# Kernel tuning notes

Hardware: AMD Instinct MI355X
Metric: run time of the kernel (lower is better)

## Reference

```python
import jax, jax.numpy as jnp
import numpy as np

EMBED_DIM = 256
N_HEADS = 1
NORM_FACTOR = float(np.sqrt(EMBED_DIM / N_HEADS))


def setup_inputs() -> dict:
    key = jax.random.key(0)
    ks = jax.random.split(key, 7)
    B, S, E = 4, 4096, EMBED_DIM
    scale = 1.0 / np.sqrt(E)
    x = jax.random.normal(ks[0], (B, S, E), dtype=jnp.float32)
    Wq = jax.random.normal(ks[1], (E, E), dtype=jnp.float32) * scale
    bq = jax.random.normal(ks[2], (E,), dtype=jnp.float32) * 0.01
    Wk = jax.random.normal(ks[3], (E, E), dtype=jnp.float32) * scale
    bk = jax.random.normal(ks[4], (E,), dtype=jnp.float32) * 0.01
    Wv = jax.random.normal(ks[5], (E, E), dtype=jnp.float32) * scale
    bv = jax.random.normal(ks[6], (E,), dtype=jnp.float32) * 0.01
    return {"x": x, "Wq": Wq, "bq": bq, "Wk": Wk, "bk": bk, "Wv": Wv, "bv": bv}


def reference(x, Wq, bq, Wk, bk, Wv, bv):
    # Linear projections (torch Linear: x @ W.T + b; W here stored as [in, out]-equivalent square)
    q = x @ Wq + bq  # [B, S, E]
    k = x @ Wk + bk  # [B, S, E]
    v = x @ Wv + bv  # [B, S, E]
    # Full attention scores [B, S, S], scaled by sqrt(embed_dim / n_heads)
    attn_scores = jnp.einsum('bse,bte->bst', q, k) / NORM_FACTOR
    attn_dist = jax.nn.softmax(attn_scores, axis=-1)
    pooled = jnp.einsum('bst,bte->bse', attn_dist, v)  # [B, S, E]
    return pooled.mean(axis=1, keepdims=True)  # [B, 1, E]
```

## Files before the change

kernel.cpp:

```cpp
#include <hip/hip_runtime.h>
#include <hip/hip_fp8.h>
#include <stdint.h>

#define SS 4096
#define EE 256
#define C2 0.0901684400555602f
#define SCALE1 0x7F7F7F7F
#define ZMAX 8.5f

typedef __bf16 bf16x8 __attribute__((ext_vector_type(8)));
typedef float  f32x4  __attribute__((ext_vector_type(4)));
typedef float  f32x2  __attribute__((ext_vector_type(2)));
typedef int    i32x8  __attribute__((ext_vector_type(8)));

#if __has_builtin(__builtin_amdgcn_exp2f)
#define EXP2(x) __builtin_amdgcn_exp2f(x)
#else
#define EXP2(x) exp2f(x)
#endif
#if __has_builtin(__builtin_amdgcn_rcpf)
#define RCP(x) __builtin_amdgcn_rcpf(x)
#else
#define RCP(x) (1.0f / (x))
#endif

__device__ __forceinline__ uint16_t bf16_rn(float f) {
  uint32_t u = __float_as_uint(f);
  uint32_t r = (u + 0x7fffu + ((u >> 16) & 1u)) >> 16;
  return (uint16_t)r;
}
__device__ __forceinline__ float bf2f(uint16_t h) {
  return __uint_as_float(((uint32_t)h) << 16);
}
__device__ __forceinline__ bf16x8 pack_bf8(float4 a, float4 b) {
  union { bf16x8 v; uint16_t u[8]; } r;
  r.u[0] = bf16_rn(a.x); r.u[1] = bf16_rn(a.y);
  r.u[2] = bf16_rn(a.z); r.u[3] = bf16_rn(a.w);
  r.u[4] = bf16_rn(b.x); r.u[5] = bf16_rn(b.y);
  r.u[6] = bf16_rn(b.z); r.u[7] = bf16_rn(b.w);
  return r.v;
}
__device__ __forceinline__ uint8_t f32_to_e4m3(float x) {
#if __has_builtin(__builtin_amdgcn_cvt_pk_fp8_f32)
  return (uint8_t)(__builtin_amdgcn_cvt_pk_fp8_f32(x, 0.f, 0, false) & 0xff);
#else
  __hip_fp8_e4m3 h(x);
  return (uint8_t)h.__x;
#endif
}
__device__ __forceinline__ uint32_t pack4_e4m3(float a, float b, float c, float d) {
#if __has_builtin(__builtin_amdgcn_cvt_pk_fp8_f32)
  int v = __builtin_amdgcn_cvt_pk_fp8_f32(a, b, 0, false);
  v = __builtin_amdgcn_cvt_pk_fp8_f32(c, d, v, true);
  return (uint32_t)v;
#else
  return (uint32_t)f32_to_e4m3(a) | ((uint32_t)f32_to_e4m3(b) << 8) |
         ((uint32_t)f32_to_e4m3(c) << 16) | ((uint32_t)f32_to_e4m3(d) << 24);
#endif
}
__device__ __forceinline__ float e4m3_f32(uint32_t u) {
  uint32_t bits = ((u & 0x80u) << 24) | ((u & 0x7fu) << 20);
  return __uint_as_float(bits) * 0x1p+120f;
}
__device__ __forceinline__ void decode_fma4(uint32_t w, float rv, float* acc) {
#if __has_builtin(__builtin_amdgcn_cvt_pk_f32_fp8)
  f32x2 lo = __builtin_amdgcn_cvt_pk_f32_fp8((int)w, false);
  f32x2 hi = __builtin_amdgcn_cvt_pk_f32_fp8((int)w, true);
  acc[0] += rv * lo[0]; acc[1] += rv * lo[1];
  acc[2] += rv * hi[0]; acc[3] += rv * hi[1];
#else
  acc[0] += rv * e4m3_f32(w & 0xffu);
  acc[1] += rv * e4m3_f32((w >> 8) & 0xffu);
  acc[2] += rv * e4m3_f32((w >> 16) & 0xffu);
  acc[3] += rv * e4m3_f32(w >> 24);
#endif
}

__device__ __forceinline__ f32x4 mfma16(bf16x8 a, bf16x8 b, f32x4 c) {
  return __builtin_amdgcn_mfma_f32_16x16x32_bf16(a, b, c, 0, 0, 0);
}
__device__ __forceinline__ f32x4 mfma128(i32x8 a, i32x8 b, f32x4 c) {
  return __builtin_amdgcn_mfma_scale_f32_16x16x128_f8f6f4(
      a, b, c, 0 , 0 , 0, SCALE1, 0, SCALE1);
}
__device__ __forceinline__ void pin8(i32x8& v) {
  asm volatile("" : "+v"(v));
}

template<int R>
__device__ __forceinline__ void stage_tile(const uint16_t* gsrc, char* lds, int tid) {
  constexpr int NPER = (R * 32) / 256;
  const int wave = tid >> 6;
  #pragma unroll
  for (int c = 0; c < NPER; ++c) {
    int chunk = c * 256 + tid;
    int r = chunk >> 5;
    int ccl = (chunk & 31) ^ (r & 31);
    const char* gp = (const char*)gsrc + (r * 32 + ccl) * 16;
    char* lp = lds + (c * 256 + wave * 64) * 16;
    __builtin_amdgcn_global_load_lds(
        (const __attribute__((address_space(1))) uint32_t*)(uintptr_t)gp,
        (__attribute__((address_space(3))) uint32_t*)(uintptr_t)lp,
        16, 0, 0);
  }
}
__device__ __forceinline__ bf16x8 read_frag(const char* lds, int row, int cc) {
  int ccp = cc ^ (row & 31);
  return *(const bf16x8*)(lds + (row * 32 + ccp) * 16);
}

__global__ void prep_kernel(const float* __restrict__ Wq, const float* __restrict__ Wk,
                            const float* __restrict__ Wv, uint16_t* __restrict__ wt,
                            float* __restrict__ zbase, float* __restrict__ out) {
  __shared__ float t[64][65];
  const int bid = blockIdx.x, tid = threadIdx.x;
  if (bid >= 48) {
    int idx = (bid - 48) * 256 + tid;
    float4 z = {0.f, 0.f, 0.f, 0.f};
    if (idx < 8192) ((float4*)zbase)[idx] = z;
    else ((float4*)out)[idx - 8192] = z;
    return;
  }
  const int mat = bid >> 4, tt = bid & 15;
  const int ib = (tt >> 2) * 64, ob = (tt & 3) * 64;
  const float* W = (mat == 0) ? Wq : (mat == 1) ? Wk : Wv;
  #pragma unroll
  for (int p = 0; p < 4; ++p) {
    int idx = p * 256 + tid;
    int r = idx >> 4, c4 = idx & 15;
    float4 f = *(const float4*)&W[(size_t)(ib + r) * 256 + ob + c4 * 4];
    t[r][c4 * 4 + 0] = f.x; t[r][c4 * 4 + 1] = f.y;
    t[r][c4 * 4 + 2] = f.z; t[r][c4 * 4 + 3] = f.w;
  }
  __syncthreads();
  #pragma unroll
  for (int p = 0; p < 4; ++p) {
    int idx = p * 256 + tid;
    int o = idx >> 4, i4 = idx & 15;
    ushort4 u;
    u.x = bf16_rn(t[i4 * 4 + 0][o]);
    u.y = bf16_rn(t[i4 * 4 + 1][o]);
    u.z = bf16_rn(t[i4 * 4 + 2][o]);
    u.w = bf16_rn(t[i4 * 4 + 3][o]);
    *(ushort4*)&wt[((size_t)mat * 256 + ob + o) * 256 + ib + i4 * 4] = u;
  }
}

__global__ __launch_bounds__(256, 2) void qkv_kernel(
    const float* __restrict__ x, const uint16_t* __restrict__ wt,
    const float* __restrict__ bq, const float* __restrict__ bk, const float* __restrict__ bv,
    uint8_t* __restrict__ q8, uint8_t* __restrict__ k8, uint16_t* __restrict__ vo) {
  __shared__ char wsm[2][32768];
  const int tid = threadIdx.x;
  const int lane = tid & 63, wave = tid >> 6, quad = lane >> 4, lr = lane & 15;
  const int m0 = (blockIdx.x >> 2) * 128;
  const int cchunk = blockIdx.x & 3;
  stage_tile<64>(wt + (size_t)(cchunk * 192) * 256, wsm[0], tid);
  const float* ab = x + (size_t)(m0 + wave * 32) * EE;
  bf16x8 a[2][8];
  #pragma unroll
  for (int ms = 0; ms < 2; ++ms)
    #pragma unroll
    for (int f = 0; f < 8; ++f) {
      const float* rp = ab + (size_t)(ms * 16 + lr) * EE + f * 32 + quad * 8;
      a[ms][f] = pack_bf8(*(const float4*)rp, *(const float4*)(rp + 4));
    }
  for (int nc = 0; nc < 3; ++nc) {
    __syncthreads();
    if (nc < 2)
      stage_tile<64>(wt + (size_t)(cchunk * 192 + (nc + 1) * 64) * 256, wsm[(nc + 1) & 1], tid);
    const char* tile = wsm[nc & 1];
    #pragma unroll
    for (int nt = 0; nt < 4; ++nt) {
      const int eg0 = cchunk * 192 + nc * 64 + nt * 16;
      const int mat = eg0 >> 8;
      const int e = (eg0 & 255) + lr;
      const float* bias = (mat == 0) ? bq : (mat == 1) ? bk : bv;
      bf16x8 bf[8];
      #pragma unroll
      for (int f = 0; f < 8; ++f) bf[f] = read_frag(tile, nt * 16 + lr, f * 4 + quad);
      f32x4 acc[2] = {};
      #pragma unroll
      for (int f = 0; f < 8; ++f)
        #pragma unroll
        for (int ms = 0; ms < 2; ++ms)
          acc[ms] = mfma16(a[ms][f], bf[f], acc[ms]);
      const float bsv = bias[e];
      #pragma unroll
      for (int ms = 0; ms < 2; ++ms)
        #pragma unroll
        for (int r = 0; r < 4; ++r) {
          int row = m0 + wave * 32 + ms * 16 + quad * 4 + r;
          float vl = acc[ms][r] + bsv;
          if (mat == 2)      vo[(size_t)row * EE + e] = bf16_rn(vl);
          else if (mat == 1) k8[(size_t)row * EE + e] = f32_to_e4m3(vl);
          else               q8[(size_t)row * EE + e] = f32_to_e4m3(vl);
        }
    }
  }
}

__global__ __launch_bounds__(256, 3) void scores_pl_kernel(
    const uint8_t* __restrict__ q8, const uint8_t* __restrict__ k8,
    uint8_t* __restrict__ p8, float* __restrict__ lacc) {
  __shared__ float lsh[256];
  const int tid = threadIdx.x;
  const int lane = tid & 63, wave = tid >> 6, quad = lane >> 4, lr = lane & 15;
  const int idx = blockIdx.x;
  const int b = idx >> 8, rem = idx & 255, kblk = rem >> 4, sch = rem & 15;
  const uint8_t* kb = k8 + (size_t)(b * SS + kblk * 256 + wave * 64) * EE;
  const uint8_t* qw = q8 + (size_t)(b * SS + sch * 256) * EE;
  lsh[tid] = 0.f;
  const uint8_t* kr = kb + (size_t)lr * EE + quad * 32;
  i32x8 a00 = *(const i32x8*)(kr + 0 * 16 * EE);
  i32x8 a01 = *(const i32x8*)(kr + 0 * 16 * EE + 128);
  i32x8 a10 = *(const i32x8*)(kr + 1 * 16 * EE);
  i32x8 a11 = *(const i32x8*)(kr + 1 * 16 * EE + 128);
  i32x8 a20 = *(const i32x8*)(kr + 2 * 16 * EE);
  i32x8 a21 = *(const i32x8*)(kr + 2 * 16 * EE + 128);
  i32x8 a30 = *(const i32x8*)(kr + 3 * 16 * EE);
  i32x8 a31 = *(const i32x8*)(kr + 3 * 16 * EE + 128);
  pin8(a00); pin8(a01); pin8(a10); pin8(a11);
  pin8(a20); pin8(a21); pin8(a30); pin8(a31);
  const size_t chunkbase = ((size_t)((b * 16 + sch) * 16 + kblk)) << 16;
  uint8_t* pst = p8 + chunkbase + (size_t)(wave * 16) * 1024 + (size_t)lane * 16;
  __syncthreads();
  #pragma unroll
  for (int it = 0; it < 4; ++it) {
    #pragma unroll
    for (int nt = 0; nt < 4; ++nt) {
      const uint8_t* qrow = qw + (size_t)(it * 64 + nt * 16 + lr) * EE;
      i32x8 bf0 = *(const i32x8*)(qrow + quad * 32);
      i32x8 bf1 = *(const i32x8*)(qrow + 128 + quad * 32);
      f32x4 acc[4] = {};
      acc[0] = mfma128(a00, bf0, acc[0]); acc[0] = mfma128(a01, bf1, acc[0]);
      acc[1] = mfma128(a10, bf0, acc[1]); acc[1] = mfma128(a11, bf1, acc[1]);
      acc[2] = mfma128(a20, bf0, acc[2]); acc[2] = mfma128(a21, bf1, acc[2]);
      acc[3] = mfma128(a30, bf0, acc[3]); acc[3] = mfma128(a31, bf1, acc[3]);
      const int sloc = it * 64 + nt * 16 + lr;
      float lpart = 0.f;
      uint32_t pw[4];
      #pragma unroll
      for (int ms = 0; ms < 4; ++ms) {
        float e0 = EXP2(fminf(acc[ms][0] * C2, ZMAX));
        float e1 = EXP2(fminf(acc[ms][1] * C2, ZMAX));
        float e2 = EXP2(fminf(acc[ms][2] * C2, ZMAX));
        float e3 = EXP2(fminf(acc[ms][3] * C2, ZMAX));
        lpart += (e0 + e1) + (e2 + e3);
        pw[ms] = pack4_e4m3(e0, e1, e2, e3);
      }
      uint4 w4; w4.x = pw[0]; w4.y = pw[1]; w4.z = pw[2]; w4.w = pw[3];
      *(uint4*)(pst + (size_t)(it * 4 + nt) * 1024) = w4;
      lpart += __shfl_xor(lpart, 16, 64);
      lpart += __shfl_xor(lpart, 32, 64);
      if (quad == 0) atomicAdd(&lsh[sloc], lpart);
    }
  }
  __syncthreads();
  atomicAdd(&lacc[b * SS + sch * 256 + tid], lsh[tid]);
}

__global__ __launch_bounds__(256) void wsum_kernel(
    const uint8_t* __restrict__ p8, const float* __restrict__ lacc,
    float* __restrict__ wacc) {
  __shared__ float rls[256];
  const int tid = threadIdx.x;
  const int idx = blockIdx.x;
  const int b = idx >> 8, rem = idx & 255, kblk = rem >> 4, sch = rem & 15;
  rls[tid] = RCP(lacc[b * SS + sch * 256 + tid]);
  __syncthreads();
  const int lane = tid & 63, wave_w = tid >> 6, lr = tid & 15;
  const size_t chunkbase = ((size_t)((b * 16 + sch) * 16 + kblk)) << 16;
  const uint8_t* pp = p8 + chunkbase + (size_t)(wave_w * 16) * 1024 + (size_t)lane * 16;
  float acc[16];
  #pragma unroll
  for (int i = 0; i < 16; ++i) acc[i] = 0.f;
  #pragma unroll
  for (int itnt = 0; itnt < 16; ++itnt) {
    uint4 pv = *(const uint4*)(pp + (size_t)itnt * 1024);
    float rv = rls[(itnt >> 2) * 64 + (itnt & 3) * 16 + lr];
    decode_fma4(pv.x, rv, acc + 0);
    decode_fma4(pv.y, rv, acc + 4);
    decode_fma4(pv.z, rv, acc + 8);
    decode_fma4(pv.w, rv, acc + 12);
  }
  #pragma unroll
  for (int d = 1; d < 16; d <<= 1)
    #pragma unroll
    for (int i = 0; i < 16; ++i)
      acc[i] += __shfl_xor(acc[i], d, 64);
  if (lr == 0) {
    float* wp = wacc + b * SS + kblk * 256 + wave_w * 64 + (lane >> 4) * 4;
    #pragma unroll
    for (int ms = 0; ms < 4; ++ms)
      #pragma unroll
      for (int r = 0; r < 4; ++r)
        atomicAdd(&wp[ms * 16 + r], acc[ms * 4 + r]);
  }
}

__global__ void pool_kernel(const float* __restrict__ wvec, const uint16_t* __restrict__ v,
                            float* __restrict__ out) {
  __shared__ float red[4][256];
  const int b = blockIdx.x >> 6, tc = blockIdx.x & 63;
  const int tq = threadIdx.x >> 6, eg = threadIdx.x & 63;
  float acc[4] = {0.f, 0.f, 0.f, 0.f};
  const float* wp = wvec + b * SS + tc * 64;
  const uint16_t* vp = v + (size_t)(b * SS + tc * 64) * EE + eg * 4;
  #pragma unroll
  for (int t = 0; t < 16; ++t) {
    int row = t * 4 + tq;
    float wv = wp[row];
    ushort4 x4 = *(const ushort4*)(vp + (size_t)row * EE);
    acc[0] += wv * bf2f(x4.x);
    acc[1] += wv * bf2f(x4.y);
    acc[2] += wv * bf2f(x4.z);
    acc[3] += wv * bf2f(x4.w);
  }
  #pragma unroll
  for (int j = 0; j < 4; ++j) red[tq][eg * 4 + j] = acc[j];
  __syncthreads();
  if (tq == 0) {
    const float inv = 1.0f / 4096.0f;
    #pragma unroll
    for (int j = 0; j < 4; ++j) {
      float s = red[0][eg * 4 + j] + red[1][eg * 4 + j] +
                red[2][eg * 4 + j] + red[3][eg * 4 + j];
      atomicAdd(&out[b * 256 + eg * 4 + j], s * inv);
    }
  }
}

extern "C" void kernel_launch(void* const* d_in, const int* in_sizes, int n_in,
                              void* d_out, int out_size, void* d_ws, size_t ws_size,
                              hipStream_t stream) {
  const float* x  = (const float*)d_in[0];
  const float* Wq = (const float*)d_in[1];
  const float* bq = (const float*)d_in[2];
  const float* Wk = (const float*)d_in[3];
  const float* bk = (const float*)d_in[4];
  const float* Wv = (const float*)d_in[5];
  const float* bv = (const float*)d_in[6];

  char* ws = (char*)d_ws;
  uint8_t*  q8    = (uint8_t*)(ws);
  uint8_t*  k8    = (uint8_t*)(ws + 4194304);
  uint16_t* vb    = (uint16_t*)(ws + 8388608);
  uint16_t* wt    = (uint16_t*)(ws + 16777216);
  float*    l_arr = (float*)(ws + 17170432);
  float*    w_arr = (float*)(ws + 17235968);
  uint8_t*  p8    = (uint8_t*)(ws + 33554432);
  float* out      = (float*)d_out;

  prep_kernel<<<81, 256, 0, stream>>>(Wq, Wk, Wv, wt, l_arr, out);
  qkv_kernel<<<512, 256, 0, stream>>>(x, wt, bq, bk, bv, q8, k8, vb);
  scores_pl_kernel<<<1024, 256, 0, stream>>>(q8, k8, p8, l_arr);
  wsum_kernel<<<1024, 256, 0, stream>>>(p8, l_arr, w_arr);
  pool_kernel<<<256, 256, 0, stream>>>(w_arr, vb, out);
}
```

Baseline: 162.4 us.

## Halve key-block tile per block to double grid and raise occupancy

The scores and weighted-sum kernels now give each block 128 key rows instead of 256, so each wave holds 32 keys of fp8 fragments in registers instead of 64. The grid doubles to 2048 blocks, launch bounds rise to 5 blocks per SM, and the P-tile layout in workspace is rebuilt to match. Probability stores become nontemporal 8-byte writes. The aim is more parallelism and latency hiding, at the cost of loading each Q tile twice as often and issuing twice as many row-sum atomics.

Measured after the change: 185.0 us. 13.9% more time.

```diff
diff --git a/kernel.cpp b/kernel.cpp
--- a/kernel.cpp
+++ b/kernel.cpp
@@ -200,30 +200,25 @@
   }
 }
 
-__global__ __launch_bounds__(256, 3) void scores_pl_kernel(
+__global__ __launch_bounds__(256, 5) void scores_pl_kernel(
     const uint8_t* __restrict__ q8, const uint8_t* __restrict__ k8,
     uint8_t* __restrict__ p8, float* __restrict__ lacc) {
   __shared__ float lsh[256];
   const int tid = threadIdx.x;
   const int lane = tid & 63, wave = tid >> 6, quad = lane >> 4, lr = lane & 15;
   const int idx = blockIdx.x;
-  const int b = idx >> 8, rem = idx & 255, kblk = rem >> 4, sch = rem & 15;
-  const uint8_t* kb = k8 + (size_t)(b * SS + kblk * 256 + wave * 64) * EE;
+  const int b = idx >> 9, rem = idx & 511, kblk = rem >> 4, sch = rem & 15;
+  const uint8_t* kb = k8 + (size_t)(b * SS + kblk * 128 + wave * 32) * EE;
   const uint8_t* qw = q8 + (size_t)(b * SS + sch * 256) * EE;
   lsh[tid] = 0.f;
   const uint8_t* kr = kb + (size_t)lr * EE + quad * 32;
-  i32x8 a00 = *(const i32x8*)(kr + 0 * 16 * EE);
-  i32x8 a01 = *(const i32x8*)(kr + 0 * 16 * EE + 128);
-  i32x8 a10 = *(const i32x8*)(kr + 1 * 16 * EE);
-  i32x8 a11 = *(const i32x8*)(kr + 1 * 16 * EE + 128);
-  i32x8 a20 = *(const i32x8*)(kr + 2 * 16 * EE);
-  i32x8 a21 = *(const i32x8*)(kr + 2 * 16 * EE + 128);
-  i32x8 a30 = *(const i32x8*)(kr + 3 * 16 * EE);
-  i32x8 a31 = *(const i32x8*)(kr + 3 * 16 * EE + 128);
+  i32x8 a00 = *(const i32x8*)(kr);
+  i32x8 a01 = *(const i32x8*)(kr + 128);
+  i32x8 a10 = *(const i32x8*)(kr + 16 * EE);
+  i32x8 a11 = *(const i32x8*)(kr + 16 * EE + 128);
   pin8(a00); pin8(a01); pin8(a10); pin8(a11);
-  pin8(a20); pin8(a21); pin8(a30); pin8(a31);
-  const size_t chunkbase = ((size_t)((b * 16 + sch) * 16 + kblk)) << 16;
-  uint8_t* pst = p8 + chunkbase + (size_t)(wave * 16) * 1024 + (size_t)lane * 16;
+  const size_t chunkbase = ((size_t)((b * 16 + sch) * 32 + kblk)) << 15;
+  uint8_t* pst = p8 + chunkbase + (size_t)wave * 8192 + (size_t)lane * 8;
   __syncthreads();
   #pragma unroll
   for (int it = 0; it < 4; ++it) {
@@ -232,25 +227,24 @@
       const uint8_t* qrow = qw + (size_t)(it * 64 + nt * 16 + lr) * EE;
       i32x8 bf0 = *(const i32x8*)(qrow + quad * 32);
       i32x8 bf1 = *(const i32x8*)(qrow + 128 + quad * 32);
-      f32x4 acc[4] = {};
-      acc[0] = mfma128(a00, bf0, acc[0]); acc[0] = mfma128(a01, bf1, acc[0]);
-      acc[1] = mfma128(a10, bf0, acc[1]); acc[1] = mfma128(a11, bf1, acc[1]);
-      acc[2] = mfma128(a20, bf0, acc[2]); acc[2] = mfma128(a21, bf1, acc[2]);
-      acc[3] = mfma128(a30, bf0, acc[3]); acc[3] = mfma128(a31, bf1, acc[3]);
+      f32x4 acc0 = {}, acc1 = {};
+      acc0 = mfma128(a00, bf0, acc0); acc0 = mfma128(a01, bf1, acc0);
+      acc1 = mfma128(a10, bf0, acc1); acc1 = mfma128(a11, bf1, acc1);
       const int sloc = it * 64 + nt * 16 + lr;
-      float lpart = 0.f;
-      uint32_t pw[4];
-      #pragma unroll
-      for (int ms = 0; ms < 4; ++ms) {
-        float e0 = EXP2(fminf(acc[ms][0] * C2, ZMAX));
-        float e1 = EXP2(fminf(acc[ms][1] * C2, ZMAX));
-        float e2 = EXP2(fminf(acc[ms][2] * C2, ZMAX));
-        float e3 = EXP2(fminf(acc[ms][3] * C2, ZMAX));
-        lpart += (e0 + e1) + (e2 + e3);
-        pw[ms] = pack4_e4m3(e0, e1, e2, e3);
-      }
-      uint4 w4; w4.x = pw[0]; w4.y = pw[1]; w4.z = pw[2]; w4.w = pw[3];
-      *(uint4*)(pst + (size_t)(it * 4 + nt) * 1024) = w4;
+      float e00 = EXP2(fminf(acc0[0] * C2, ZMAX));
+      float e01 = EXP2(fminf(acc0[1] * C2, ZMAX));
+      float e02 = EXP2(fminf(acc0[2] * C2, ZMAX));
+      float e03 = EXP2(fminf(acc0[3] * C2, ZMAX));
+      float e10 = EXP2(fminf(acc1[0] * C2, ZMAX));
+      float e11 = EXP2(fminf(acc1[1] * C2, ZMAX));
+      float e12 = EXP2(fminf(acc1[2] * C2, ZMAX));
+      float e13 = EXP2(fminf(acc1[3] * C2, ZMAX));
+      float lpart = ((e00 + e01) + (e02 + e03)) + ((e10 + e11) + (e12 + e13));
+      union { uint32_t w[2]; unsigned long long u; } pv;
+      pv.w[0] = pack4_e4m3(e00, e01, e02, e03);
+      pv.w[1] = pack4_e4m3(e10, e11, e12, e13);
+      __builtin_nontemporal_store(
+          pv.u, (unsigned long long*)(pst + (size_t)(it * 4 + nt) * 512));
       lpart += __shfl_xor(lpart, 16, 64);
       lpart += __shfl_xor(lpart, 32, 64);
       if (quad == 0) atomicAdd(&lsh[sloc], lpart);
@@ -266,33 +260,31 @@
   __shared__ float rls[256];
   const int tid = threadIdx.x;
   const int idx = blockIdx.x;
-  const int b = idx >> 8, rem = idx & 255, kblk = rem >> 4, sch = rem & 15;
+  const int b = idx >> 9, rem = idx & 511, kblk = rem >> 4, sch = rem & 15;
   rls[tid] = RCP(lacc[b * SS + sch * 256 + tid]);
   __syncthreads();
   const int lane = tid & 63, wave_w = tid >> 6, lr = tid & 15;
-  const size_t chunkbase = ((size_t)((b * 16 + sch) * 16 + kblk)) << 16;
-  const uint8_t* pp = p8 + chunkbase + (size_t)(wave_w * 16) * 1024 + (size_t)lane * 16;
-  float acc[16];
-  #pragma unroll
-  for (int i = 0; i < 16; ++i) acc[i] = 0.f;
-  #pragma unroll
-  for (int itnt = 0; itnt < 16; ++itnt) {
-    uint4 pv = *(const uint4*)(pp + (size_t)itnt * 1024);
-    float rv = rls[(itnt >> 2) * 64 + (itnt & 3) * 16 + lr];
+  const size_t chunkbase = ((size_t)((b * 16 + sch) * 32 + kblk)) << 15;
+  const uint8_t* pp = p8 + chunkbase + (size_t)wave_w * 8192 + (size_t)lane * 8;
+  float acc[8];
+  #pragma unroll
+  for (int i = 0; i < 8; ++i) acc[i] = 0.f;
+  #pragma unroll
+  for (int step = 0; step < 16; ++step) {
+    uint2 pv = *(const uint2*)(pp + (size_t)step * 512);
+    float rv = rls[(step >> 2) * 64 + (step & 3) * 16 + lr];
     decode_fma4(pv.x, rv, acc + 0);
     decode_fma4(pv.y, rv, acc + 4);
-    decode_fma4(pv.z, rv, acc + 8);
-    decode_fma4(pv.w, rv, acc + 12);
   }
   #pragma unroll
   for (int d = 1; d < 16; d <<= 1)
     #pragma unroll
-    for (int i = 0; i < 16; ++i)
+    for (int i = 0; i < 8; ++i)
       acc[i] += __shfl_xor(acc[i], d, 64);
   if (lr == 0) {
-    float* wp = wacc + b * SS + kblk * 256 + wave_w * 64 + (lane >> 4) * 4;
-    #pragma unroll
-    for (int ms = 0; ms < 4; ++ms)
+    float* wp = wacc + b * SS + kblk * 128 + wave_w * 32 + (lane >> 4) * 4;
+    #pragma unroll
+    for (int ms = 0; ms < 2; ++ms)
       #pragma unroll
       for (int r = 0; r < 4; ++r)
         atomicAdd(&wp[ms * 16 + r], acc[ms * 4 + r]);
@@ -354,7 +346,7 @@
 
   prep_kernel<<<81, 256, 0, stream>>>(Wq, Wk, Wv, wt, l_arr, out);
   qkv_kernel<<<512, 256, 0, stream>>>(x, wt, bq, bk, bv, q8, k8, vb);
-  scores_pl_kernel<<<1024, 256, 0, stream>>>(q8, k8, p8, l_arr);
-  wsum_kernel<<<1024, 256, 0, stream>>>(p8, l_arr, w_arr);
+  scores_pl_kernel<<<2048, 256, 0, stream>>>(q8, k8, p8, l_arr);
+  wsum_kernel<<<2048, 256, 0, stream>>>(p8, l_arr, w_arr);
   pool_kernel<<<256, 256, 0, stream>>>(w_arr, vb, out);
 }
```
